# Kernel tuning notes

Measured on AMD Instinct MI355X. Metric: run time of the kernel, lower is better.

The kernel has to match this reference:

```python
import jax, jax.numpy as jnp
import numpy as np

N_QUBITS = 10
DEPTH = 2
CNOT_PATTERN = [(i, i + 1) for i in range(N_QUBITS - 1)] + [(N_QUBITS - 1, 0)]

def _signs(n):
    # Pauli-Z eigenvalue (+1/-1) of each basis state for each wire; wire 0 = MSB
    idx = np.arange(2 ** n)
    bits = (idx[:, None] >> np.arange(n - 1, -1, -1)[None, :]) & 1
    return jnp.asarray(1.0 - 2.0 * bits, jnp.float32)  # [2^n, n]

SIGNS = _signs(N_QUBITS)

def _apply_rx(s, theta, wire):
    # s: [B, 2,2,...,2] complex; RX(theta) = [[c, -i s],[-i s, c]], c=cos(theta/2)
    s0 = jnp.take(s, 0, axis=wire + 1)
    s1 = jnp.take(s, 1, axis=wire + 1)
    c = jnp.cos(theta * 0.5)
    sn = jnp.sin(theta * 0.5)
    if c.ndim:  # per-batch angle -> broadcast over remaining wire axes
        shp = (-1,) + (1,) * (s0.ndim - 1)
        c = c.reshape(shp)
        sn = sn.reshape(shp)
    return jnp.stack([c * s0 - 1j * sn * s1, -1j * sn * s0 + c * s1], axis=wire + 1)

def _apply_cnot(s, src, tgt):
    # flip target wire on the src=1 subspace (X gate == flip of the size-2 axis)
    s0 = jnp.take(s, 0, axis=src + 1)
    s1 = jnp.take(s, 1, axis=src + 1)
    t_ax = tgt + 1 - (1 if tgt > src else 0)  # target axis after removing src axis
    s1 = jnp.flip(s1, axis=t_ax)
    return jnp.stack([s0, s1], axis=src + 1)

def _qgate(x, rx_params):
    # x: [B, n_qubits] data angles -> PauliZ expectations [B, n_qubits]
    B = x.shape[0]
    n = N_QUBITS
    s = jnp.zeros((B, 2 ** n), jnp.complex64).at[:, 0].set(1.0)
    s = s.reshape((B,) + (2,) * n)
    for w in range(n):
        s = _apply_rx(s, x[:, w], w)
    for _ in range(DEPTH):
        for w in range(n):
            s = _apply_rx(s, rx_params[w], w)
        for src, tgt in CNOT_PATTERN:
            s = _apply_cnot(s, src, tgt)
    probs = jnp.abs(s.reshape(B, -1)) ** 2  # [B, 2^n]
    return probs @ SIGNS  # [B, n]


def setup_inputs():
    key = jax.random.key(0)
    ks = jax.random.split(key, 10)
    T, B, D, H = 256, 256, 128, N_QUBITS
    fan_in = D + H
    sc = 1.0 / np.sqrt(fan_in)
    def lin(k1, k2):
        W = jax.random.uniform(k1, (H, fan_in), jnp.float32, -sc, sc)
        b = jax.random.uniform(k2, (H,), jnp.float32, -sc, sc)
        return W, b
    inputs = jax.random.normal(ks[0], (T, B, D), jnp.float32)
    rx_params = jax.random.normal(ks[1], (H,), jnp.float32)
    Wf, bf = lin(ks[2], ks[3])
    Wi, bi = lin(ks[4], ks[5])
    Wg, bg = lin(ks[6], ks[7])
    Wo, bo = lin(ks[8], ks[9])
    return dict(inputs=inputs, rx_params=rx_params, Wf=Wf, bf=bf, Wi=Wi, bi=bi,
                Wg=Wg, bg=bg, Wo=Wo, bo=bo)


def reference(inputs, rx_params, Wf, bf, Wi, bi, Wg, bg, Wo, bo):
    T, B, _ = inputs.shape
    H = N_QUBITS
    def step(carry, x_t):
        hx, cx = carry
        comb = jnp.concatenate([x_t, hx], axis=1)  # [B, D+H]
        f = jax.nn.sigmoid(_qgate(comb @ Wf.T + bf, rx_params))
        i = jax.nn.sigmoid(_qgate(comb @ Wi.T + bi, rx_params))
        g = jnp.tanh(_qgate(comb @ Wg.T + bg, rx_params))
        o = jax.nn.sigmoid(_qgate(comb @ Wo.T + bo, rx_params))
        cx = f * cx + i * g
        hx = o * jnp.tanh(cx)
        return (hx, cx), hx
    h0 = jnp.zeros((B, H), inputs.dtype)
    c0 = jnp.zeros((B, H), inputs.dtype)
    (hT, cT), ys = jax.lax.scan(step, (h0, c0), inputs)
    return ys, hT, cT
```

## Files before the change

kernel.cpp:

```cpp
#include <hip/hip_runtime.h>
#include <math.h>

#define T_STEPS 256
#define BATCH   256
#define DDIM    128
#define NH      10

typedef float v2f __attribute__((ext_vector_type(2)));
__device__ __forceinline__ v2f sp(float x){ v2f r; r.x = x; r.y = x; return r; }
#define PKFMA(a,b,c) __builtin_elementwise_fma((a),(b),(c))

template<int CTRL, int RMASK, int BMASK>
__device__ __forceinline__ float dppz(float x){
  return __int_as_float(__builtin_amdgcn_update_dpp(
      0, __float_as_int(x), CTRL, RMASK, BMASK, true));
}
__device__ __forceinline__ float red63(float v){
  v += dppz<0x111, 0xF, 0xF>(v);
  v += dppz<0x112, 0xF, 0xF>(v);
  v += dppz<0x114, 0xF, 0xE>(v);
  v += dppz<0x118, 0xF, 0xC>(v);
  v += dppz<0x142, 0xA, 0xF>(v);
  v += dppz<0x143, 0xC, 0xF>(v);
  return v;
}
__device__ __forceinline__ float rdlane(float v, int l){
  return __int_as_float(__builtin_amdgcn_readlane(__float_as_int(v), l));
}

template<int CTRL,int RMASK,int BMASK>
__device__ __forceinline__ float lad_add(float v){ return v + dppz<CTRL,RMASK,BMASK>(v); }
template<int CTRL,int RMASK,int BMASK>
__device__ __forceinline__ float lad_sub(float v){ return dppz<CTRL,RMASK,BMASK>(v) - v; }
#define LAD0_A(v) lad_add<0x111,0xF,0xF>(v)
#define LAD0_S(v) lad_sub<0x111,0xF,0xF>(v)
#define LAD1_A(v) lad_add<0x112,0xF,0xF>(v)
#define LAD1_S(v) lad_sub<0x112,0xF,0xF>(v)
#define LAD2_A(v) lad_add<0x114,0xF,0xE>(v)
#define LAD2_S(v) lad_sub<0x114,0xF,0xE>(v)
#define LAD3_A(v) lad_add<0x118,0xF,0xC>(v)
#define LAD3_S(v) lad_sub<0x118,0xF,0xC>(v)
#define LAD4_A(v) lad_add<0x142,0xA,0xF>(v)
#define LAD4_S(v) lad_sub<0x142,0xA,0xF>(v)
#define LAD5_A(v) lad_add<0x143,0xC,0xF>(v)
#define LAD5_S(v) lad_sub<0x143,0xC,0xF>(v)

__device__ __forceinline__ float dsx32(float x){ return __shfl_xor(x, 32, 64); }
__device__ __forceinline__ float dsx16(float x){
  return __int_as_float(__builtin_amdgcn_ds_swizzle(__float_as_int(x), 0x401F));
}
__device__ __forceinline__ float dsx8(float x){
  return __int_as_float(__builtin_amdgcn_ds_swizzle(__float_as_int(x), 0x201F));
}
__device__ __forceinline__ float dsx4(float x){
  return __int_as_float(__builtin_amdgcn_ds_swizzle(__float_as_int(x), 0x101F));
}
__device__ __forceinline__ float dsx2(float x){
  return __int_as_float(__builtin_amdgcn_ds_swizzle(__float_as_int(x), 0x081F));
}
__device__ __forceinline__ float dsx1(float x){
  return __int_as_float(__builtin_amdgcn_ds_swizzle(__float_as_int(x), 0x041F));
}

#define NK 4

#define RX_LANE_T(FETCH, tv)                                                   \
  { const v2f tt_ = sp(tv), nt_ = sp(-(tv));                                   \
    _Pragma("unroll")                                                          \
    for (int k = 0; k < NK; ++k){                                              \
      v2f oa, ob;                                                              \
      oa.x = FETCH(RE[k].x); oa.y = FETCH(RE[k].y);                            \
      ob.x = FETCH(IM[k].x); ob.y = FETCH(IM[k].y);                            \
      RE[k] = PKFMA(tt_, ob, RE[k]);                                           \
      IM[k] = PKFMA(nt_, oa, IM[k]);                                           \
    } }

template<int XB>
__device__ __forceinline__ void rx_reg_t(float tv, v2f* RE, v2f* IM){
  const v2f tt = sp(tv), nt = sp(-tv);
  v2f oR[NK], oI[NK];
  #pragma unroll
  for (int k = 0; k < NK; ++k){ oR[k] = RE[k]; oI[k] = IM[k]; }
  #pragma unroll
  for (int k = 0; k < NK; ++k){
    RE[k] = PKFMA(tt, oI[k ^ XB], RE[k]);
    IM[k] = PKFMA(nt, oR[k ^ XB], IM[k]);
  }
}
__device__ __forceinline__ void rx_reg9_t(float tv, v2f* RE, v2f* IM){
  const v2f tt = sp(tv), nt = sp(-tv);
  #pragma unroll
  for (int k = 0; k < NK; ++k){
    v2f oa = __builtin_shufflevector(RE[k], RE[k], 1, 0);
    v2f ob = __builtin_shufflevector(IM[k], IM[k], 1, 0);
    RE[k] = PKFMA(tt, ob, RE[k]);
    IM[k] = PKFMA(nt, oa, IM[k]);
  }
}

__device__ __forceinline__ void xdots(float xa, float xb,
                                      const v2f* WA, const v2f* WB, float* s){
  v2f xav = sp(xa), xbv = sp(xb);
  v2f p0 = PKFMA(xav, WA[0], xbv * WB[0]);
  v2f p1 = PKFMA(xav, WA[1], xbv * WB[1]);
  v2f p2 = PKFMA(xav, WA[2], xbv * WB[2]);
  s[0] = red63(p0.x); s[1] = red63(p0.y);
  s[2] = red63(p1.x); s[3] = red63(p1.y);
  s[4] = red63(p2.x);
}

__global__ void __launch_bounds__(512)
__attribute__((amdgpu_waves_per_eu(2)))
qlstm_kernel(const float* __restrict__ inp, const float* __restrict__ rxp,
             const float* __restrict__ Wf, const float* __restrict__ bf,
             const float* __restrict__ Wi, const float* __restrict__ bi,
             const float* __restrict__ Wg, const float* __restrict__ bg,
             const float* __restrict__ Wo, const float* __restrict__ bo,
             float* __restrict__ out)
{
  const int b    = blockIdx.x;
  const int tid  = threadIdx.x;
  const int wv   = tid >> 6;
  const int g    = wv >> 1;
  const int half = wv & 1;
  const int lane = tid & 63;

  __shared__ float4 partv[2][64];
  __shared__ float xpub_s[4][16];
  ((float*)partv)[tid] = 0.f;

  const float* Wp = (g == 0) ? Wf : (g == 1) ? Wi : (g == 2) ? Wg : Wo;
  const float* bp = (g == 0) ? bf : (g == 1) ? bi : (g == 2) ? bg : bo;

  const float WSC = 0.07957747154594767f;

  const int wbase = half * 5;
  v2f WA[3], WB[3];
  float bq[5];
  #pragma unroll
  for (int k = 0; k < 5; ++k) bq[k] = WSC * (bp[wbase + k] + rxp[wbase + k]);
  #pragma unroll
  for (int j = 0; j < 3; ++j){
    const int w0 = wbase + 2*j, w1 = wbase + 2*j + 1;
    WA[j].x = WSC * Wp[w0*138 + lane];
    WB[j].x = WSC * Wp[w0*138 + 64 + lane];
    if (2*j + 1 < 5){
      WA[j].y = WSC * Wp[w1*138 + lane];
      WB[j].y = WSC * Wp[w1*138 + 64 + lane];
    } else { WA[j].y = 0.f; WB[j].y = 0.f; }
  }
  float wCT[NH];
  {
    const int row = (lane < NH) ? lane : 0;
    #pragma unroll
    for (int j = 0; j < NH; ++j){
      float v = WSC * Wp[row*138 + 128 + j];
      wCT[j] = (lane < NH) ? v : 0.f;
    }
  }

  float tq[NH];
  float PC = 1.f;
  #pragma unroll
  for (int w = 0; w < NH; ++w){
    float th = 0.5f * rxp[w];
    float cw = cosf(th), sw = sinf(th);
    PC *= cw;
    tq[w] = sw / cw;
  }

  const int l5 = (lane>>5)&1, l4 = (lane>>4)&1, l3 = (lane>>3)&1;
  const int l2 = (lane>>2)&1, l1 = (lane>>1)&1, l0 = lane&1;
  const int pb2 = l4^l3, pb3 = l3^l2, pb4 = l2^l1, pb5 = l1^l0;
  const int a0 = l5, a1 = l5^l4;
  const int a6w = l0 ^ half;
  const int n_base = pb2 + pb3 + pb4 + pb5 + a6w;

  v2f CRE[NK], CIM[NK], D6RE[NK], D6IM[NK];
  #pragma unroll
  for (int r = 0; r < 2*NK; ++r){
    const int R0 = r&1, R1 = (r>>1)&1, R2 = (r>>2)&1;
    int k = (n_base + (a0^R0) + (a1^R0) + (half^R2) + (R2^R1) + (R1^R0)) & 3;
    float cr = (k==0) ? PC : (k==2) ? -PC : 0.f;
    float ci = (k==1) ? -PC : (k==3) ? PC : 0.f;
    float sg6 = ((l0 ^ R2) & 1) ? tq[6] : -tq[6];
    float dre = sg6 * ci;
    float dim = -sg6 * cr;
    if (R0){ CRE[r>>1].y = cr;  CIM[r>>1].y = ci;
             D6RE[r>>1].y = dre; D6IM[r>>1].y = dim; }
    else   { CRE[r>>1].x = cr;  CIM[r>>1].x = ci;
             D6RE[r>>1].x = dre; D6IM[r>>1].x = dim; }
  }

  const float sig = (lane == 0 || lane >= 6) ? -1.f : 1.f;

  float h = 0.f, c = 0.f;

  const float* x0 = inp + (size_t)b * DDIM;
  float xa = x0[lane];
  float xb = x0[64 + lane];

  {
    float sx[5];
    xdots(xa, xb, WA, WB, sx);
    if (lane == 63){
      #pragma unroll
      for (int k = 0; k < 5; ++k) xpub_s[g][wbase + k] = sx[k] + bq[k];
    }
  }
  __syncthreads();

  #pragma unroll 1
  for (int t = 0; t < T_STEPS; ++t){
    if (t + 1 < T_STEPS){
      const float* nx = inp + ((size_t)(t+1) * BATCH + b) * DDIM;
      xa = nx[lane];
      xb = nx[64 + lane];
    }

    float cs[NH], sn[NH];
    {
      float xr = xpub_s[g][lane & 15];
      float hdA = rdlane(h, 0) * wCT[0];
      float hdB = rdlane(h, 1) * wCT[1];
      hdA = fmaf(rdlane(h, 2), wCT[2], hdA);
      hdB = fmaf(rdlane(h, 3), wCT[3], hdB);
      hdA = fmaf(rdlane(h, 4), wCT[4], hdA);
      hdB = fmaf(rdlane(h, 5), wCT[5], hdB);
      hdA = fmaf(rdlane(h, 6), wCT[6], hdA);
      hdB = fmaf(rdlane(h, 7), wCT[7], hdB);
      hdA = fmaf(rdlane(h, 8), wCT[8], hdA);
      hdB = fmaf(rdlane(h, 9), wCT[9], hdB);
      float th = xr + (hdA + hdB);
      float cA = __builtin_amdgcn_cosf(th);
      float sA = __builtin_amdgcn_sinf(th);
      #pragma unroll
      for (int w = 0; w < NH; ++w){
        cs[w] = rdlane(cA, w);
        sn[w] = rdlane(sA, w);
      }
    }

    float f2 = pb2 ? sn[2] : cs[2];
    float f3 = pb3 ? sn[3] : cs[3];
    float f4 = pb4 ? sn[4] : cs[4];
    float f5 = pb5 ? sn[5] : cs[5];
    float m2345b = (f2*f3)*(f4*f5);
    float w6o = a6w ? sn[6] : cs[6];
    float w6p = a6w ? cs[6] : sn[6];
    float mo = m2345b * w6o;
    float mp = m2345b * w6p;

    float q0 = (a0 ? sn[0] : cs[0]) * (a1 ? sn[1] : cs[1]);
    float q1 = (a0 ? cs[0] : sn[0]) * (a1 ? cs[1] : sn[1]);
    v2f ZZ; ZZ.x = mo * q0; ZZ.y = mo * q1;
    v2f ZP; ZP.x = mp * q0; ZP.y = mp * q1;

    float u7  = half ? sn[7] : cs[7];
    float u7b = half ? cs[7] : sn[7];
    float t78[4];
    t78[0] = u7  * cs[8];
    t78[1] = u7  * sn[8];
    t78[2] = u7b * sn[8];
    t78[3] = u7b * cs[8];

    v2f s9a; s9a.x = cs[9]; s9a.y = sn[9];
    v2f s9b; s9b.x = sn[9]; s9b.y = cs[9];

    v2f RE[NK], IM[NK];
    #pragma unroll
    for (int k = 0; k < NK; ++k){
      v2f s9v = (k & 1) ? s9b : s9a;
      v2f M  = (sp(t78[k])     * s9v) * ZZ;
      v2f Mp = (sp(t78[k ^ 3]) * s9v) * ZP;
      RE[k] = PKFMA(Mp, D6RE[k], M * CRE[k]);
      IM[k] = PKFMA(Mp, D6IM[k], M * CIM[k]);
    }

    RX_LANE_T(dsx32, tq[0])
    RX_LANE_T(dsx16, tq[1])
    RX_LANE_T(dsx8,  tq[2])
    RX_LANE_T(dsx4,  tq[3])
    RX_LANE_T(dsx2,  tq[4])
    RX_LANE_T(dsx1,  tq[5])
    rx_reg_t<2>(tq[7], RE, IM);
    rx_reg_t<1>(tq[8], RE, IM);
    rx_reg9_t  (tq[9], RE, IM);

    float sx[5];
    xdots(xa, xb, WA, WB, sx);

    v2f Pk[NK];
    #pragma unroll
    for (int k = 0; k < NK; ++k) Pk[k] = PKFMA(RE[k], RE[k], IM[k] * IM[k]);
    float A0 = Pk[0].x + Pk[0].y, A1 = Pk[1].x + Pk[1].y;
    float A2 = Pk[2].x + Pk[2].y, A3 = Pk[3].x + Pk[3].y;
    float B0 = Pk[0].x - Pk[0].y, B1 = Pk[1].x - Pk[1].y;
    float B2 = Pk[2].x - Pk[2].y, B3 = Pk[3].x - Pk[3].y;
    float su = A0 + A1, sv = A2 + A3;
    float tot = su + sv;
    float q4  = su - sv;
    float q6  = (A0 - A1) - (A2 - A3);
    float q7  = (B0 - B1) - (B2 - B3);

    float a0p = LAD0_A(tot);
    float a0m = LAD0_S(tot);
    float b1pp = LAD1_A(a0p);
    float b1pm = LAD1_S(a0p);
    float b1mm = LAD1_S(a0m);
    float c2ppp = LAD2_A(b1pp);
    float c2ppm = LAD2_S(b1pp);
    float c2pmm = LAD2_S(b1pm);
    float c2mmm = LAD2_S(b1mm);
    float d1 = LAD3_A(c2ppp);
    float d2 = LAD3_S(c2ppp);
    float d3 = LAD3_S(c2ppm);
    float d4 = LAD3_S(c2pmm);
    float d5 = LAD3_S(c2mmm);
    float P1 = LAD5_S(LAD4_S(d1));
    float P2 = LAD5_S(LAD4_S(d2));
    float P3 = LAD5_S(LAD4_S(d3));
    float P4 = LAD5_S(LAD4_S(d4));
    float P5 = LAD5_S(LAD4_S(d5));
    float e = LAD0_S(q7);
    e = LAD1_S(e); e = LAD2_S(e); e = LAD3_S(e); e = LAD4_S(e);
    float P9 = LAD5_S(e);
    float P0 = LAD5_A(e);
    float f_ = LAD0_S(q4);
    f_ = LAD1_S(f_); f_ = LAD2_S(f_); f_ = LAD3_S(f_); f_ = LAD4_S(f_);
    float P7 = LAD5_S(f_);
    float g_ = LAD0_S(q6);
    g_ = LAD1_S(g_); g_ = LAD2_S(g_); g_ = LAD3_S(g_); g_ = LAD4_S(g_);
    float P8 = LAD5_S(g_);

    if (lane == 63){
      float vals[10] = {P0,P1,P2,P3,P4,P5,P5,P7,P8,P9};
      #pragma unroll
      for (int j = 0; j < 10; ++j)
        ((float*)&partv[half][j])[g] = vals[j];
      #pragma unroll
      for (int k = 0; k < 5; ++k)
        xpub_s[g][wbase + k] = sx[k] + bq[k];
    }
    __syncthreads();

    float4 eL = partv[0][lane];
    float4 eH = partv[1][lane];
    float E0 = fmaf(sig, eH.x, eL.x);
    float E1 = fmaf(sig, eH.y, eL.y);
    float E2 = fmaf(sig, eH.z, eL.z);
    float E3 = fmaf(sig, eH.w, eL.w);
    float fv = 1.f / (1.f + __expf(-E0));
    float iv = 1.f / (1.f + __expf(-E1));
    float e2g = __expf(2.f * E2);
    float gv = (e2g - 1.f) / (e2g + 1.f);
    float ov = 1.f / (1.f + __expf(-E3));
    c = fmaf(fv, c, iv * gv);
    float e2c = __expf(2.f * c);
    h = ov * ((e2c - 1.f) / (e2c + 1.f));

    if (wv == 0 && lane < NH)
      out[((size_t)t * BATCH + b) * NH + lane] = h;
  }

  if (wv == 0 && lane < NH){
    const size_t ysN = (size_t)T_STEPS * BATCH * NH;
    out[ysN + (size_t)b * NH + lane]                      = h;
    out[ysN + (size_t)BATCH * NH + (size_t)b * NH + lane] = c;
  }
}

extern "C" void kernel_launch(void* const* d_in, const int* in_sizes, int n_in,
                              void* d_out, int out_size, void* d_ws, size_t ws_size,
                              hipStream_t stream)
{
  qlstm_kernel<<<BATCH, 512, 0, stream>>>(
      (const float*)d_in[0], (const float*)d_in[1],
      (const float*)d_in[2], (const float*)d_in[3],
      (const float*)d_in[4], (const float*)d_in[5],
      (const float*)d_in[6], (const float*)d_in[7],
      (const float*)d_in[8], (const float*)d_in[9],
      (float*)d_out);
}
```

Baseline: 753.5 us.

## Compute sin via shifted cos lanes, bpermute gather, merged butterfly reductions

```diff
diff --git a/kernel.cpp b/kernel.cpp
--- a/kernel.cpp
+++ b/kernel.cpp
@@ -14,15 +14,6 @@
 __device__ __forceinline__ float dppz(float x){
   return __int_as_float(__builtin_amdgcn_update_dpp(
       0, __float_as_int(x), CTRL, RMASK, BMASK, true));
-}
-__device__ __forceinline__ float red63(float v){
-  v += dppz<0x111, 0xF, 0xF>(v);
-  v += dppz<0x112, 0xF, 0xF>(v);
-  v += dppz<0x114, 0xF, 0xE>(v);
-  v += dppz<0x118, 0xF, 0xC>(v);
-  v += dppz<0x142, 0xA, 0xF>(v);
-  v += dppz<0x143, 0xC, 0xF>(v);
-  return v;
 }
 __device__ __forceinline__ float rdlane(float v, int l){
   return __int_as_float(__builtin_amdgcn_readlane(__float_as_int(v), l));
@@ -61,6 +52,9 @@
 __device__ __forceinline__ float dsx1(float x){
   return __int_as_float(__builtin_amdgcn_ds_swizzle(__float_as_int(x), 0x041F));
 }
+__device__ __forceinline__ float bperm(int addr, float v){
+  return __int_as_float(__builtin_amdgcn_ds_bpermute(addr, __float_as_int(v)));
+}
 
 #define NK 4
 
@@ -98,15 +92,35 @@
   }
 }
 
-__device__ __forceinline__ void xdots(float xa, float xb,
-                                      const v2f* WA, const v2f* WB, float* s){
+__device__ __forceinline__ void xdots5(float xa, float xb,
+                                       const v2f* WA, const v2f* WB,
+                                       int l5, int l4, int l3, float* s){
   v2f xav = sp(xa), xbv = sp(xb);
   v2f p0 = PKFMA(xav, WA[0], xbv * WB[0]);
   v2f p1 = PKFMA(xav, WA[1], xbv * WB[1]);
   v2f p2 = PKFMA(xav, WA[2], xbv * WB[2]);
-  s[0] = red63(p0.x); s[1] = red63(p0.y);
-  s[2] = red63(p1.x); s[3] = red63(p1.y);
-  s[4] = red63(p2.x);
+  float a = p0.x + dsx32(p0.x);
+  float bv = p0.y + dsx32(p0.y);
+  float c = p1.x + dsx32(p1.x);
+  float d = p1.y + dsx32(p1.y);
+  float e = p2.x + dsx32(p2.x);
+  float m1 = l5 ? bv : a;
+  float m2 = l5 ? d : c;
+  m1 += dsx16(m1);
+  m2 += dsx16(m2);
+  e  += dsx16(e);
+  float n1 = l4 ? m2 : m1;
+  n1 += dsx8(n1);
+  e  += dsx8(e);
+  float p = l3 ? e : n1;
+  p += dsx4(p);
+  p += dsx2(p);
+  p += dsx1(p);
+  s[0] = rdlane(p, 0);
+  s[1] = rdlane(p, 32);
+  s[2] = rdlane(p, 16);
+  s[3] = rdlane(p, 48);
+  s[4] = rdlane(p, 8);
 }
 
 __global__ void __launch_bounds__(512)
@@ -128,6 +142,7 @@
   __shared__ float4 partv[2][64];
   __shared__ float xpub_s[4][16];
   ((float*)partv)[tid] = 0.f;
+  if (tid < 64) ((float*)xpub_s)[tid] = 0.f;
 
   const float* Wp = (g == 0) ? Wf : (g == 1) ? Wi : (g == 2) ? Wg : Wo;
   const float* bp = (g == 0) ? bf : (g == 1) ? bi : (g == 2) ? bg : bo;
@@ -149,15 +164,17 @@
       WB[j].y = WSC * Wp[w1*138 + 64 + lane];
     } else { WA[j].y = 0.f; WB[j].y = 0.f; }
   }
+  const int trigAct = (lane < NH) || (lane >= 16 && lane < 16 + NH);
   float wCT[NH];
   {
-    const int row = (lane < NH) ? lane : 0;
+    const int row = trigAct ? (lane & 15) : 0;
     #pragma unroll
     for (int j = 0; j < NH; ++j){
       float v = WSC * Wp[row*138 + 128 + j];
-      wCT[j] = (lane < NH) ? v : 0.f;
-    }
-  }
+      wCT[j] = trigAct ? v : 0.f;
+    }
+  }
+  const float shift = ((lane >> 4) & 1) ? -0.25f : 0.f;
 
   float tq[NH];
   float PC = 1.f;
@@ -175,6 +192,17 @@
   const int a0 = l5, a1 = l5^l4;
   const int a6w = l0 ^ half;
   const int n_base = pb2 + pb3 + pb4 + pb5 + a6w;
+
+  const int adF2  = 4*(2 + 16*pb2);
+  const int adF3  = 4*(3 + 16*pb3);
+  const int adF4  = 4*(4 + 16*pb4);
+  const int adF5  = 4*(5 + 16*pb5);
+  const int adW6o = 4*(6 + 16*a6w);
+  const int adW6p = 4*(6 + 16*(a6w^1));
+  const int adQ0a = 4*(0 + 16*a0);
+  const int adQ0b = 4*(1 + 16*a1);
+  const int adQ1a = 4*(0 + 16*(a0^1));
+  const int adQ1b = 4*(1 + 16*(a1^1));
 
   v2f CRE[NK], CIM[NK], D6RE[NK], D6IM[NK];
   #pragma unroll
@@ -202,7 +230,7 @@
 
   {
     float sx[5];
-    xdots(xa, xb, WA, WB, sx);
+    xdots5(xa, xb, WA, WB, l5, l4, l3, sx);
     if (lane == 63){
       #pragma unroll
       for (int k = 0; k < 5; ++k) xpub_s[g][wbase + k] = sx[k] + bq[k];
@@ -218,7 +246,7 @@
       xb = nx[64 + lane];
     }
 
-    float cs[NH], sn[NH];
+    float cA;
     {
       float xr = xpub_s[g][lane & 15];
       float hdA = rdlane(h, 0) * wCT[0];
@@ -231,41 +259,40 @@
       hdB = fmaf(rdlane(h, 7), wCT[7], hdB);
       hdA = fmaf(rdlane(h, 8), wCT[8], hdA);
       hdB = fmaf(rdlane(h, 9), wCT[9], hdB);
-      float th = xr + (hdA + hdB);
-      float cA = __builtin_amdgcn_cosf(th);
-      float sA = __builtin_amdgcn_sinf(th);
-      #pragma unroll
-      for (int w = 0; w < NH; ++w){
-        cs[w] = rdlane(cA, w);
-        sn[w] = rdlane(sA, w);
-      }
-    }
-
-    float f2 = pb2 ? sn[2] : cs[2];
-    float f3 = pb3 ? sn[3] : cs[3];
-    float f4 = pb4 ? sn[4] : cs[4];
-    float f5 = pb5 ? sn[5] : cs[5];
+      float th = (xr + (hdA + hdB)) + shift;
+      cA = __builtin_amdgcn_cosf(th);
+    }
+
+    float f2  = bperm(adF2,  cA);
+    float f3  = bperm(adF3,  cA);
+    float f4  = bperm(adF4,  cA);
+    float f5  = bperm(adF5,  cA);
+    float w6o = bperm(adW6o, cA);
+    float w6p = bperm(adW6p, cA);
+    float q0a = bperm(adQ0a, cA);
+    float q0b = bperm(adQ0b, cA);
+    float q1a = bperm(adQ1a, cA);
+    float q1b = bperm(adQ1b, cA);
     float m2345b = (f2*f3)*(f4*f5);
-    float w6o = a6w ? sn[6] : cs[6];
-    float w6p = a6w ? cs[6] : sn[6];
     float mo = m2345b * w6o;
     float mp = m2345b * w6p;
-
-    float q0 = (a0 ? sn[0] : cs[0]) * (a1 ? sn[1] : cs[1]);
-    float q1 = (a0 ? cs[0] : sn[0]) * (a1 ? cs[1] : sn[1]);
+    float q0 = q0a*q0b, q1 = q1a*q1b;
     v2f ZZ; ZZ.x = mo * q0; ZZ.y = mo * q1;
     v2f ZP; ZP.x = mp * q0; ZP.y = mp * q1;
 
-    float u7  = half ? sn[7] : cs[7];
-    float u7b = half ? cs[7] : sn[7];
+    float u7  = rdlane(cA, 7 + 16*half);
+    float u7b = rdlane(cA, 23 - 16*half);
+    float c8  = rdlane(cA, 8);
+    float s8  = rdlane(cA, 24);
+    float c9  = rdlane(cA, 9);
+    float s9  = rdlane(cA, 25);
     float t78[4];
-    t78[0] = u7  * cs[8];
-    t78[1] = u7  * sn[8];
-    t78[2] = u7b * sn[8];
-    t78[3] = u7b * cs[8];
-
-    v2f s9a; s9a.x = cs[9]; s9a.y = sn[9];
-    v2f s9b; s9b.x = sn[9]; s9b.y = cs[9];
+    t78[0] = u7  * c8;
+    t78[1] = u7  * s8;
+    t78[2] = u7b * s8;
+    t78[3] = u7b * c8;
+    v2f s9a; s9a.x = c9; s9a.y = s9;
+    v2f s9b; s9b.x = s9; s9b.y = c9;
 
     v2f RE[NK], IM[NK];
     #pragma unroll
@@ -278,17 +305,17 @@
     }
 
     RX_LANE_T(dsx32, tq[0])
+    rx_reg_t<2>(tq[7], RE, IM);
     RX_LANE_T(dsx16, tq[1])
+    rx_reg_t<1>(tq[8], RE, IM);
     RX_LANE_T(dsx8,  tq[2])
+    rx_reg9_t  (tq[9], RE, IM);
     RX_LANE_T(dsx4,  tq[3])
     RX_LANE_T(dsx2,  tq[4])
     RX_LANE_T(dsx1,  tq[5])
-    rx_reg_t<2>(tq[7], RE, IM);
-    rx_reg_t<1>(tq[8], RE, IM);
-    rx_reg9_t  (tq[9], RE, IM);
 
     float sx[5];
-    xdots(xa, xb, WA, WB, sx);
+    xdots5(xa, xb, WA, WB, l5, l4, l3, sx);
 
     v2f Pk[NK];
     #pragma unroll
```

After: 763.2 us. Within noise of the previous version (+1.3%).
